# Kernel optimization log

Measured on AMD Instinct MI355X. Metric: run time of the kernel, lower is better.

The kernel has to match this reference:

```python
import jax, jax.numpy as jnp
import numpy as np

N = 100000      # num nodes == input_dim (featureless RGCN)
S = 50          # support (num relations)
B = 30          # num_bases
OUT = 16        # output_dim
E = 20000       # edges per relation


def setup_inputs() -> dict:
    key = jax.random.key(0)
    k1, k2, k3, k4, k5, k6 = jax.random.split(key, 6)
    features = jax.random.normal(k1, (N, 1), dtype=jnp.float32)
    src = jax.random.randint(k2, (S, E), 0, N, dtype=jnp.int32)
    dst = jax.random.randint(k3, (S, E), 0, N, dtype=jnp.int32)
    vals = jax.random.uniform(k4, (S, E), dtype=jnp.float32)
    # learned params (xavier-ish scale)
    W = jax.random.normal(k5, (N * B, OUT), dtype=jnp.float32) * (2.0 / (N * B + OUT)) ** 0.5
    W_comp = jax.random.normal(k6, (S, B), dtype=jnp.float32) * (2.0 / (S + B)) ** 0.5
    return {"features": features, "src": src, "dst": dst, "vals": vals, "W": W, "W_comp": W_comp}


def reference(features, src, dst, vals, W, W_comp):
    n = features.shape[0]  # == N (featureless: input_dim == num_nodes)
    # Basis decomposition, exactly as torch:
    # V = W_comp @ W.reshape(B, N, OUT).permute(1, 0, 2)  -> [N, S, OUT]
    Wb = W.reshape(B, n, OUT).transpose(1, 0, 2)          # [N, B, OUT]
    V = jnp.einsum('sb,nbo->nso', W_comp, Wb)             # [N, S, OUT]
    # torch reshape (support*input_dim, OUT): row k = node*S + rel (node-major)
    V2 = V.reshape(S * n, OUT)                            # [S*N, OUT]
    # supports is block-concat sparse [N, S*N], column = rel*N + node (relation-major)
    # output = supports @ V2: for edge (i=src, j=dst) in relation r:
    #   out[i] += val * V2[r*N + j]
    gather_idx = (jnp.arange(S, dtype=src.dtype)[:, None] * n + dst).reshape(-1)  # [S*E]
    msgs = V2[gather_idx] * vals.reshape(-1, 1)           # [S*E, OUT]
    out = jax.ops.segment_sum(msgs, src.reshape(-1), num_segments=n)  # [N, OUT]
    # featureless dropout scaling: tmp = dropout(ones(N)); p=0 -> identity
    return jax.nn.relu(out)
```

## Files before the change

### kernel.cpp

```cpp
#include <hip/hip_runtime.h>

constexpr int S_REL = 50;
constexpr int B_BASES = 30;
constexpr int OUT_DIM = 16;
constexpr int NXCD = 8;
constexpr int EDGES_PER_BLOCK = 64;

__global__ __launch_bounds__(256) void relu_inplace_kernel(float4* __restrict__ p, int n4) {
    int i = blockIdx.x * blockDim.x + threadIdx.x;
    int stride = gridDim.x * blockDim.x;
    for (; i < n4; i += stride) {
        float4 v = p[i];
        v.x = fmaxf(v.x, 0.f);
        v.y = fmaxf(v.y, 0.f);
        v.z = fmaxf(v.z, 0.f);
        v.w = fmaxf(v.w, 0.f);
        p[i] = v;
    }
}

__global__ __launch_bounds__(256) void rgcn_edge_kernel(
    const int* __restrict__ src, const int* __restrict__ dst,
    const float* __restrict__ vals, const float* __restrict__ W,
    const float* __restrict__ Wcomp, float* __restrict__ out,
    int N, int E, int nEdges, int chunksPerXcd, int nChunks) {
    __shared__ float wc[S_REL * B_BASES];
    for (int i = threadIdx.x; i < S_REL * B_BASES; i += blockDim.x)
        wc[i] = Wcomp[i];
    __syncthreads();

    const int x = blockIdx.x % NXCD;
    const int j = blockIdx.x / NXCD;
    const int chunk = x * chunksPerXcd + j;
    if (chunk >= nChunks) return;

    const int edge = chunk * EDGES_PER_BLOCK + (threadIdx.x >> 2);
    const int o4 = (threadIdx.x & 3) * 4;
    if (edge >= nEdges) return;

    const int r = edge / E;
    const int d = dst[edge];
    const int s = src[edge];
    const float v = vals[edge];

    const int k = r * N + d;
    const int node = k / S_REL;
    const int rel = k - node * S_REL;

    const float* wp = W + (size_t)node * OUT_DIM + o4;
    const size_t bstride = (size_t)N * OUT_DIM;
    const float* wcr = wc + rel * B_BASES;

    float c[B_BASES];
#pragma unroll
    for (int b = 0; b < B_BASES; ++b) c[b] = wcr[b];

    float4 acc = make_float4(0.f, 0.f, 0.f, 0.f);
#pragma unroll
    for (int b = 0; b < B_BASES; ++b) {
        float4 w4 = *reinterpret_cast<const float4*>(wp + (size_t)b * bstride);
        acc.x = fmaf(c[b], w4.x, acc.x);
        acc.y = fmaf(c[b], w4.y, acc.y);
        acc.z = fmaf(c[b], w4.z, acc.z);
        acc.w = fmaf(c[b], w4.w, acc.w);
    }

    float* op = out + (size_t)s * OUT_DIM + o4;
    atomicAdd(op + 0, v * acc.x);
    atomicAdd(op + 1, v * acc.y);
    atomicAdd(op + 2, v * acc.z);
    atomicAdd(op + 3, v * acc.w);
}

extern "C" void kernel_launch(void* const* d_in, const int* in_sizes, int n_in,
                              void* d_out, int out_size, void* d_ws, size_t ws_size,
                              hipStream_t stream) {
    const int* src = (const int*)d_in[1];
    const int* dst = (const int*)d_in[2];
    const float* vals = (const float*)d_in[3];
    const float* W = (const float*)d_in[4];
    const float* Wcomp = (const float*)d_in[5];
    float* out = (float*)d_out;

    const int N = in_sizes[0];
    const int nEdges = in_sizes[1];
    const int E = nEdges / S_REL;

    hipMemsetAsync(d_out, 0, (size_t)out_size * sizeof(float), stream);

    const int nChunks = (nEdges + EDGES_PER_BLOCK - 1) / EDGES_PER_BLOCK;
    const int chunksPerXcd = (nChunks + NXCD - 1) / NXCD;
    const int eblocks = chunksPerXcd * NXCD;
    rgcn_edge_kernel<<<eblocks, 256, 0, stream>>>(src, dst, vals, W, Wcomp, out,
                                                  N, E, nEdges, chunksPerXcd, nChunks);

    const int n4 = out_size / 4;
    int zb = (n4 + 255) / 256;
    const int rblocks = zb < 2048 ? zb : 2048;
    relu_inplace_kernel<<<rblocks, 256, 0, stream>>>((float4*)out, n4);
}
```

Before: 486.4 us.

## Replace float atomics with histogram-scan bucketing and per-node segmented reduction

Replaces per-edge float atomicAdds into the output with a CSR-style pipeline. A histogram counts edges per source node, a single-block scan builds offsets, and a gather kernel writes each edge's message into a bucketed workspace slot. A reduce kernel then sums each node's messages and applies ReLU in one pass. This removes the output memset, the float atomics and the separate ReLU pass, at the cost of five launches, a serial single-block scan over 100k nodes, and a 64 MB message buffer round trip.

```diff
diff --git a/kernel.cpp b/kernel.cpp
--- a/kernel.cpp
+++ b/kernel.cpp
@@ -11,65 +11,149 @@
     int stride = gridDim.x * blockDim.x;
     for (; i < n4; i += stride) {
         float4 v = p[i];
-        v.x = fmaxf(v.x, 0.f);
-        v.y = fmaxf(v.y, 0.f);
-        v.z = fmaxf(v.z, 0.f);
-        v.w = fmaxf(v.w, 0.f);
+        v.x = fmaxf(v.x, 0.f); v.y = fmaxf(v.y, 0.f);
+        v.z = fmaxf(v.z, 0.f); v.w = fmaxf(v.w, 0.f);
         p[i] = v;
     }
 }
 
-__global__ __launch_bounds__(256) void rgcn_edge_kernel(
+__global__ __launch_bounds__(256) void rgcn_edge_atomic_kernel(
     const int* __restrict__ src, const int* __restrict__ dst,
     const float* __restrict__ vals, const float* __restrict__ W,
     const float* __restrict__ Wcomp, float* __restrict__ out,
     int N, int E, int nEdges, int chunksPerXcd, int nChunks) {
     __shared__ float wc[S_REL * B_BASES];
-    for (int i = threadIdx.x; i < S_REL * B_BASES; i += blockDim.x)
-        wc[i] = Wcomp[i];
+    for (int i = threadIdx.x; i < S_REL * B_BASES; i += blockDim.x) wc[i] = Wcomp[i];
     __syncthreads();
-
     const int x = blockIdx.x % NXCD;
     const int j = blockIdx.x / NXCD;
     const int chunk = x * chunksPerXcd + j;
     if (chunk >= nChunks) return;
-
     const int edge = chunk * EDGES_PER_BLOCK + (threadIdx.x >> 2);
     const int o4 = (threadIdx.x & 3) * 4;
     if (edge >= nEdges) return;
-
     const int r = edge / E;
     const int d = dst[edge];
     const int s = src[edge];
     const float v = vals[edge];
-
     const int k = r * N + d;
     const int node = k / S_REL;
     const int rel = k - node * S_REL;
-
     const float* wp = W + (size_t)node * OUT_DIM + o4;
     const size_t bstride = (size_t)N * OUT_DIM;
     const float* wcr = wc + rel * B_BASES;
-
-    float c[B_BASES];
-#pragma unroll
-    for (int b = 0; b < B_BASES; ++b) c[b] = wcr[b];
-
     float4 acc = make_float4(0.f, 0.f, 0.f, 0.f);
 #pragma unroll
     for (int b = 0; b < B_BASES; ++b) {
         float4 w4 = *reinterpret_cast<const float4*>(wp + (size_t)b * bstride);
-        acc.x = fmaf(c[b], w4.x, acc.x);
-        acc.y = fmaf(c[b], w4.y, acc.y);
-        acc.z = fmaf(c[b], w4.z, acc.z);
-        acc.w = fmaf(c[b], w4.w, acc.w);
-    }
-
+        float c = wcr[b];
+        acc.x = fmaf(c, w4.x, acc.x); acc.y = fmaf(c, w4.y, acc.y);
+        acc.z = fmaf(c, w4.z, acc.z); acc.w = fmaf(c, w4.w, acc.w);
+    }
     float* op = out + (size_t)s * OUT_DIM + o4;
-    atomicAdd(op + 0, v * acc.x);
-    atomicAdd(op + 1, v * acc.y);
-    atomicAdd(op + 2, v * acc.z);
-    atomicAdd(op + 3, v * acc.w);
+    atomicAdd(op + 0, v * acc.x); atomicAdd(op + 1, v * acc.y);
+    atomicAdd(op + 2, v * acc.z); atomicAdd(op + 3, v * acc.w);
+}
+
+__global__ __launch_bounds__(256) void hist_kernel(
+    const int* __restrict__ src, unsigned* __restrict__ cnt, int nEdges) {
+    int i = blockIdx.x * blockDim.x + threadIdx.x;
+    int stride = gridDim.x * blockDim.x;
+    for (; i < nEdges; i += stride) atomicAdd(&cnt[src[i]], 1u);
+}
+
+__global__ __launch_bounds__(1024) void scan_kernel(
+    const unsigned* __restrict__ cnt, unsigned* __restrict__ offs,
+    unsigned* __restrict__ cur, int N) {
+    __shared__ unsigned sums[1024];
+    const int t = threadIdx.x;
+    const int per = (N + 1023) / 1024;
+    const int lo = t * per;
+    const int hi = (lo + per < N) ? lo + per : N;
+    unsigned s = 0;
+    for (int i = lo; i < hi; ++i) s += cnt[i];
+    sums[t] = s;
+    __syncthreads();
+    for (int d = 1; d < 1024; d <<= 1) {
+        unsigned v = (t >= d) ? sums[t - d] : 0u;
+        __syncthreads();
+        sums[t] += v;
+        __syncthreads();
+    }
+    unsigned base = (t == 0) ? 0u : sums[t - 1];
+    for (int i = lo; i < hi; ++i) {
+        unsigned c = cnt[i];
+        offs[i] = base;
+        cur[i] = base;
+        base += c;
+    }
+    if (t == 1023) offs[N] = sums[1023];
+}
+
+__global__ __launch_bounds__(256) void gather_kernel(
+    const int* __restrict__ src, const int* __restrict__ dst,
+    const float* __restrict__ vals, const float* __restrict__ W,
+    const float* __restrict__ Wcomp, float* __restrict__ msgs,
+    unsigned* __restrict__ cur,
+    int N, int E, int nEdges, int chunksPerXcd, int nChunks) {
+    __shared__ float wc[S_REL * B_BASES];
+    for (int i = threadIdx.x; i < S_REL * B_BASES; i += blockDim.x) wc[i] = Wcomp[i];
+    __syncthreads();
+
+    const int x = blockIdx.x % NXCD;
+    const int j = blockIdx.x / NXCD;
+    const int chunk = x * chunksPerXcd + j;
+    if (chunk >= nChunks) return;
+    const int edge = chunk * EDGES_PER_BLOCK + (threadIdx.x >> 2);
+    const int o4 = (threadIdx.x & 3) * 4;
+    if (edge >= nEdges) return;
+
+    const int r = edge / E;
+    const int d = dst[edge];
+    const int s = src[edge];
+    const float v = vals[edge];
+    const int k = r * N + d;
+    const int node = k / S_REL;
+    const int rel = k - node * S_REL;
+
+    const float* wp = W + (size_t)node * OUT_DIM + o4;
+    const size_t bstride = (size_t)N * OUT_DIM;
+    const float* wcr = wc + rel * B_BASES;
+
+    float4 acc = make_float4(0.f, 0.f, 0.f, 0.f);
+#pragma unroll
+    for (int b = 0; b < B_BASES; ++b) {
+        float4 w4 = *reinterpret_cast<const float4*>(wp + (size_t)b * bstride);
+        float c = wcr[b];
+        acc.x = fmaf(c, w4.x, acc.x); acc.y = fmaf(c, w4.y, acc.y);
+        acc.z = fmaf(c, w4.z, acc.z); acc.w = fmaf(c, w4.w, acc.w);
+    }
+
+    unsigned pos = 0;
+    if ((threadIdx.x & 3) == 0) pos = atomicAdd(&cur[s], 1u);
+    pos = __shfl(pos, 0, 4);
+
+    float4* mp = reinterpret_cast<float4*>(msgs + (size_t)pos * OUT_DIM);
+    mp[threadIdx.x & 3] = make_float4(v * acc.x, v * acc.y, v * acc.z, v * acc.w);
+}
+
+__global__ __launch_bounds__(256) void reduce_kernel(
+    const float* __restrict__ msgs, const unsigned* __restrict__ offs,
+    float* __restrict__ out, int N) {
+    const int t = blockIdx.x * blockDim.x + threadIdx.x;
+    const int n = t >> 2;
+    const int q = t & 3;
+    if (n >= N) return;
+    const unsigned b = offs[n];
+    const unsigned e = offs[n + 1];
+    float4 acc = make_float4(0.f, 0.f, 0.f, 0.f);
+    for (unsigned p = b; p < e; ++p) {
+        float4 m = *reinterpret_cast<const float4*>(msgs + (size_t)p * OUT_DIM + q * 4);
+        acc.x += m.x; acc.y += m.y; acc.z += m.z; acc.w += m.w;
+    }
+    float4* op = reinterpret_cast<float4*>(out + (size_t)n * OUT_DIM);
+    op[q] = make_float4(fmaxf(acc.x, 0.f), fmaxf(acc.y, 0.f),
+                        fmaxf(acc.z, 0.f), fmaxf(acc.w, 0.f));
 }
 
 extern "C" void kernel_launch(void* const* d_in, const int* in_sizes, int n_in,
@@ -86,16 +170,38 @@
     const int nEdges = in_sizes[1];
     const int E = nEdges / S_REL;
 
-    hipMemsetAsync(d_out, 0, (size_t)out_size * sizeof(float), stream);
-
     const int nChunks = (nEdges + EDGES_PER_BLOCK - 1) / EDGES_PER_BLOCK;
     const int chunksPerXcd = (nChunks + NXCD - 1) / NXCD;
     const int eblocks = chunksPerXcd * NXCD;
-    rgcn_edge_kernel<<<eblocks, 256, 0, stream>>>(src, dst, vals, W, Wcomp, out,
-                                                  N, E, nEdges, chunksPerXcd, nChunks);
-
-    const int n4 = out_size / 4;
-    int zb = (n4 + 255) / 256;
-    const int rblocks = zb < 2048 ? zb : 2048;
-    relu_inplace_kernel<<<rblocks, 256, 0, stream>>>((float4*)out, n4);
-}
+
+    const size_t msgsBytes = (size_t)nEdges * OUT_DIM * sizeof(float);
+    const size_t needed = msgsBytes + (size_t)(3 * N + 1) * sizeof(unsigned);
+
+    if (ws_size < needed) {
+        hipMemsetAsync(d_out, 0, (size_t)out_size * sizeof(float), stream);
+        rgcn_edge_atomic_kernel<<<eblocks, 256, 0, stream>>>(
+            src, dst, vals, W, Wcomp, out, N, E, nEdges, chunksPerXcd, nChunks);
+        const int n4 = out_size / 4;
+        int zb = (n4 + 255) / 256;
+        relu_inplace_kernel<<<(zb < 2048 ? zb : 2048), 256, 0, stream>>>((float4*)out, n4);
+        return;
+    }
+
+    float* msgs = (float*)d_ws;
+    unsigned* cnt = (unsigned*)((char*)d_ws + msgsBytes);
+    unsigned* offs = cnt + N;
+    unsigned* cur = offs + N + 1;
+
+    hipMemsetAsync(cnt, 0, (size_t)N * sizeof(unsigned), stream);
+
+    int hb = (nEdges + 255) / 256;
+    hist_kernel<<<(hb < 2048 ? hb : 2048), 256, 0, stream>>>(src, cnt, nEdges);
+
+    scan_kernel<<<1, 1024, 0, stream>>>(cnt, offs, cur, N);
+
+    gather_kernel<<<eblocks, 256, 0, stream>>>(src, dst, vals, W, Wcomp, msgs, cur,
+                                               N, E, nEdges, chunksPerXcd, nChunks);
+
+    const int rblocks = (N * 4 + 255) / 256;
+    reduce_kernel<<<rblocks, 256, 0, stream>>>(msgs, offs, out, N);
+}
```

Measured after the change: 752.2 us. 54.6% more time.

## Materialize basis-combined V2 in relation chunks, then gather-scatter per edge

Applied to the files above, without the earlier changes.

Instead of recombining the 30 basis weight rows on the fly for every edge, each group of up to 10 relations now gets its dense V2 rows written to workspace by a coalesced build kernel. A separate consume kernel then gathers one 16-float row per edge and atomically adds it into the output. The goal is to replace scattered 30-way W gathers per edge with streaming reads of W. The cost is computing all N*S rows rather than only the rows edges touch, plus extra workspace writes and more kernel launches. The old fused path remains as a fallback when the workspace is too small.

```diff
diff --git a/kernel.cpp b/kernel.cpp
--- a/kernel.cpp
+++ b/kernel.cpp
@@ -3,57 +3,28 @@
 constexpr int S_REL = 50;
 constexpr int B_BASES = 30;
 constexpr int OUT_DIM = 16;
-constexpr int NXCD = 8;
-constexpr int EDGES_PER_BLOCK = 64;
 
-__global__ __launch_bounds__(256) void relu_inplace_kernel(float4* __restrict__ p, int n4) {
-    int i = blockIdx.x * blockDim.x + threadIdx.x;
-    int stride = gridDim.x * blockDim.x;
-    for (; i < n4; i += stride) {
-        float4 v = p[i];
-        v.x = fmaxf(v.x, 0.f);
-        v.y = fmaxf(v.y, 0.f);
-        v.z = fmaxf(v.z, 0.f);
-        v.w = fmaxf(v.w, 0.f);
-        p[i] = v;
-    }
-}
 
-__global__ __launch_bounds__(256) void rgcn_edge_kernel(
-    const int* __restrict__ src, const int* __restrict__ dst,
-    const float* __restrict__ vals, const float* __restrict__ W,
-    const float* __restrict__ Wcomp, float* __restrict__ out,
-    int N, int E, int nEdges, int chunksPerXcd, int nChunks) {
+__global__ __launch_bounds__(256) void build_v2_kernel(
+    const float* __restrict__ W, const float* __restrict__ Wcomp,
+    float* __restrict__ V2c, int kBase, int rows, int N) {
     __shared__ float wc[S_REL * B_BASES];
     for (int i = threadIdx.x; i < S_REL * B_BASES; i += blockDim.x)
         wc[i] = Wcomp[i];
     __syncthreads();
 
-    const int x = blockIdx.x % NXCD;
-    const int j = blockIdx.x / NXCD;
-    const int chunk = x * chunksPerXcd + j;
-    if (chunk >= nChunks) return;
+    int t = blockIdx.x * blockDim.x + threadIdx.x;
+    int idx = t >> 2;
+    int o4 = (t & 3) * 4;
+    if (idx >= rows) return;
 
-    const int edge = chunk * EDGES_PER_BLOCK + (threadIdx.x >> 2);
-    const int o4 = (threadIdx.x & 3) * 4;
-    if (edge >= nEdges) return;
-
-    const int r = edge / E;
-    const int d = dst[edge];
-    const int s = src[edge];
-    const float v = vals[edge];
-
-    const int k = r * N + d;
-    const int node = k / S_REL;
-    const int rel = k - node * S_REL;
+    int k = kBase + idx;
+    int node = k / S_REL;
+    int rel = k - node * S_REL;
 
     const float* wp = W + (size_t)node * OUT_DIM + o4;
     const size_t bstride = (size_t)N * OUT_DIM;
-    const float* wcr = wc + rel * B_BASES;
-
-    float c[B_BASES];
-#pragma unroll
-    for (int b = 0; b < B_BASES; ++b) c[b] = wcr[b];
+    const float* c = wc + rel * B_BASES;
 
     float4 acc = make_float4(0.f, 0.f, 0.f, 0.f);
 #pragma unroll
@@ -64,12 +35,80 @@
         acc.z = fmaf(c[b], w4.z, acc.z);
         acc.w = fmaf(c[b], w4.w, acc.w);
     }
+    *reinterpret_cast<float4*>(V2c + (size_t)idx * OUT_DIM + o4) = acc;
+}
 
+__global__ __launch_bounds__(256) void consume_kernel(
+    const int* __restrict__ src, const int* __restrict__ dst,
+    const float* __restrict__ vals, const float* __restrict__ V2c,
+    float* __restrict__ out,
+    int kBase, int edgeBase, int nEdgesChunk, int N, int E) {
+    int t = blockIdx.x * blockDim.x + threadIdx.x;
+    int el = t >> 4;
+    int o = t & 15;
+    if (el >= nEdgesChunk) return;
+    int edge = edgeBase + el;
+
+    int r = edge / E;
+    int d = dst[edge];
+    int s = src[edge];
+    float v = vals[edge];
+
+    int row = r * N + d - kBase;
+    float m = v * V2c[(size_t)row * OUT_DIM + o];
+    atomicAdd(out + (size_t)s * OUT_DIM + o, m);
+}
+
+__global__ __launch_bounds__(256) void relu_inplace_kernel(float4* __restrict__ p, int n4) {
+    int i = blockIdx.x * blockDim.x + threadIdx.x;
+    int stride = gridDim.x * blockDim.x;
+    for (; i < n4; i += stride) {
+        float4 v = p[i];
+        v.x = fmaxf(v.x, 0.f); v.y = fmaxf(v.y, 0.f);
+        v.z = fmaxf(v.z, 0.f); v.w = fmaxf(v.w, 0.f);
+        p[i] = v;
+    }
+}
+
+constexpr int NXCD = 8;
+constexpr int EDGES_PER_BLOCK = 64;
+
+__global__ __launch_bounds__(256) void rgcn_edge_atomic_kernel(
+    const int* __restrict__ src, const int* __restrict__ dst,
+    const float* __restrict__ vals, const float* __restrict__ W,
+    const float* __restrict__ Wcomp, float* __restrict__ out,
+    int N, int E, int nEdges, int chunksPerXcd, int nChunks) {
+    __shared__ float wc[S_REL * B_BASES];
+    for (int i = threadIdx.x; i < S_REL * B_BASES; i += blockDim.x) wc[i] = Wcomp[i];
+    __syncthreads();
+    const int x = blockIdx.x % NXCD;
+    const int j = blockIdx.x / NXCD;
+    const int chunk = x * chunksPerXcd + j;
+    if (chunk >= nChunks) return;
+    const int edge = chunk * EDGES_PER_BLOCK + (threadIdx.x >> 2);
+    const int o4 = (threadIdx.x & 3) * 4;
+    if (edge >= nEdges) return;
+    const int r = edge / E;
+    const int d = dst[edge];
+    const int s = src[edge];
+    const float v = vals[edge];
+    const int k = r * N + d;
+    const int node = k / S_REL;
+    const int rel = k - node * S_REL;
+    const float* wp = W + (size_t)node * OUT_DIM + o4;
+    const size_t bstride = (size_t)N * OUT_DIM;
+    const float* wcr = wc + rel * B_BASES;
+    float4 acc = make_float4(0.f, 0.f, 0.f, 0.f);
+#pragma unroll
+    for (int b = 0; b < B_BASES; ++b) {
+        float4 w4 = *reinterpret_cast<const float4*>(wp + (size_t)b * bstride);
+        float c = wcr[b];
+        acc.x = fmaf(c, w4.x, acc.x); acc.y = fmaf(c, w4.y, acc.y);
+        acc.z = fmaf(c, w4.z, acc.z); acc.w = fmaf(c, w4.w, acc.w);
+    }
     float* op = out + (size_t)s * OUT_DIM + o4;
-    atomicAdd(op + 0, v * acc.x);
-    atomicAdd(op + 1, v * acc.y);
-    atomicAdd(op + 2, v * acc.z);
-    atomicAdd(op + 3, v * acc.w);
+    atomicAdd(op + 0, v * acc.x); atomicAdd(op + 1, v * acc.y);
+    atomicAdd(op + 2, v * acc.z); atomicAdd(op + 3, v * acc.w);
 }
 
 extern "C" void kernel_launch(void* const* d_in, const int* in_sizes, int n_in,
@@ -88,14 +127,35 @@
 
     hipMemsetAsync(d_out, 0, (size_t)out_size * sizeof(float), stream);
 
-    const int nChunks = (nEdges + EDGES_PER_BLOCK - 1) / EDGES_PER_BLOCK;
-    const int chunksPerXcd = (nChunks + NXCD - 1) / NXCD;
-    const int eblocks = chunksPerXcd * NXCD;
-    rgcn_edge_kernel<<<eblocks, 256, 0, stream>>>(src, dst, vals, W, Wcomp, out,
-                                                  N, E, nEdges, chunksPerXcd, nChunks);
+    const size_t relBytes = (size_t)N * OUT_DIM * sizeof(float);
+    int cap = (int)(ws_size / relBytes);
+    int Rc = cap < 10 ? cap : 10;
+    if (Rc > S_REL) Rc = S_REL;
+
+    if (Rc < 1) {
+        const int nChunks = (nEdges + EDGES_PER_BLOCK - 1) / EDGES_PER_BLOCK;
+        const int chunksPerXcd = (nChunks + NXCD - 1) / NXCD;
+        rgcn_edge_atomic_kernel<<<chunksPerXcd * NXCD, 256, 0, stream>>>(
+            src, dst, vals, W, Wcomp, out, N, E, nEdges, chunksPerXcd, nChunks);
+    } else {
+        float* V2c = (float*)d_ws;
+        for (int r0 = 0; r0 < S_REL; r0 += Rc) {
+            const int rc = (r0 + Rc <= S_REL) ? Rc : (S_REL - r0);
+            const int rows = rc * N;
+            const int kBase = r0 * N;
+            const int edgeBase = r0 * E;
+            const int nEdgesChunk = rc * E;
+
+            const int bblocks = (rows * 4 + 255) / 256;
+            build_v2_kernel<<<bblocks, 256, 0, stream>>>(W, Wcomp, V2c, kBase, rows, N);
+
+            const int cblocks = (nEdgesChunk * 16 + 255) / 256;
+            consume_kernel<<<cblocks, 256, 0, stream>>>(src, dst, vals, V2c, out,
+                                                        kBase, edgeBase, nEdgesChunk, N, E);
+        }
+    }
 
     const int n4 = out_size / 4;
     int zb = (n4 + 255) / 256;
-    const int rblocks = zb < 2048 ? zb : 2048;
-    relu_inplace_kernel<<<rblocks, 256, 0, stream>>>((float4*)out, n4);
+    relu_inplace_kernel<<<(zb < 2048 ? zb : 2048), 256, 0, stream>>>((float4*)out, n4);
 }
```

Result: slower. 820.3 us (+68.6%).

## Materialize basis-combined V2 densely and replace float atomics with CSR segmented reduce

Applied to the files above, without the earlier changes.

Each call now builds the full [N*S, OUT] relation weight table with a tiled kernel that reads W once and combines the bases for all 50 relations. The per-edge 30-basis random gathers are replaced by a single 64-byte row gather. Float atomics into the output are replaced by a counting sort on src (histogram, three-stage scan, scatter of messages) and an atomic-free per-node reduction with ReLU fused in. The cost is a large dense V2 write, several small kernel launches, and a workspace requirement; if the workspace is too small the code falls back to the old atomic path.

```diff
diff --git a/kernel.cpp b/kernel.cpp
--- a/kernel.cpp
+++ b/kernel.cpp
@@ -3,6 +3,132 @@
 constexpr int S_REL = 50;
 constexpr int B_BASES = 30;
 constexpr int OUT_DIM = 16;
+constexpr int TILE_N = 32;
+
+__global__ __launch_bounds__(128) void build_v2_tiled(
+    const float4* __restrict__ W4, const float* __restrict__ Wcomp,
+    float4* __restrict__ V24, int N) {
+    __shared__ float scw[S_REL * B_BASES];
+    const int t = threadIdx.x;
+    const int nodeBase = blockIdx.x * TILE_N;
+    const int nf4 = N * 4;
+
+    for (int i = t; i < S_REL * B_BASES; i += 128) scw[i] = Wcomp[i];
+
+    float4 f[B_BASES];
+    const int off = nodeBase * 4 + t;
+#pragma unroll
+    for (int b = 0; b < B_BASES; ++b)
+        f[b] = (off < nf4) ? W4[(size_t)b * nf4 + off]
+                           : make_float4(0.f, 0.f, 0.f, 0.f);
+    __syncthreads();
+
+    const int nl = t >> 2;
+    const int o4 = t & 3;
+    const int node = nodeBase + nl;
+    if (node >= N) return;
+
+    for (int rel = 0; rel < S_REL; ++rel) {
+        const float* c = &scw[rel * B_BASES];
+        float4 a = make_float4(0.f, 0.f, 0.f, 0.f);
+#pragma unroll
+        for (int b = 0; b < B_BASES; ++b) {
+            float cb = c[b];
+            a.x = fmaf(cb, f[b].x, a.x);
+            a.y = fmaf(cb, f[b].y, a.y);
+            a.z = fmaf(cb, f[b].z, a.z);
+            a.w = fmaf(cb, f[b].w, a.w);
+        }
+        V24[((size_t)node * S_REL + rel) * 4 + o4] = a;
+    }
+}
+
+__global__ __launch_bounds__(256) void hist_kernel(
+    const int* __restrict__ src, unsigned* __restrict__ cnt, int nEdges) {
+    int i = blockIdx.x * blockDim.x + threadIdx.x;
+    int stride = gridDim.x * blockDim.x;
+    for (; i < nEdges; i += stride) atomicAdd(&cnt[src[i]], 1u);
+}
+
+__global__ __launch_bounds__(1024) void scanA_kernel(
+    const unsigned* __restrict__ cnt, unsigned* __restrict__ offs,
+    unsigned* __restrict__ bsum, int N) {
+    __shared__ unsigned s[1024];
+    const int t = threadIdx.x;
+    const int i = blockIdx.x * 1024 + t;
+    unsigned x = (i < N) ? cnt[i] : 0u;
+    s[t] = x;
+    __syncthreads();
+    for (int d = 1; d < 1024; d <<= 1) {
+        unsigned v = (t >= d) ? s[t - d] : 0u;
+        __syncthreads();
+        s[t] += v;
+        __syncthreads();
+    }
+    if (i < N) offs[i] = s[t] - x;
+    if (t == 1023) bsum[blockIdx.x] = s[1023];
+}
+
+__global__ __launch_bounds__(64) void scanB_kernel(
+    unsigned* __restrict__ bsum, unsigned* __restrict__ bofs, int nb) {
+    if (threadIdx.x == 0) {
+        unsigned run = 0;
+        for (int j = 0; j < nb; ++j) { unsigned x = bsum[j]; bofs[j] = run; run += x; }
+    }
+}
+
+__global__ __launch_bounds__(1024) void scanC_kernel(
+    unsigned* __restrict__ offs, unsigned* __restrict__ cur,
+    const unsigned* __restrict__ bofs, int N, int nEdges) {
+    const int i = blockIdx.x * 1024 + threadIdx.x;
+    if (i < N) {
+        unsigned o = offs[i] + bofs[i >> 10];
+        offs[i] = o;
+        cur[i] = o;
+    }
+    if (i == 0) offs[N] = (unsigned)nEdges;
+}
+
+__global__ __launch_bounds__(256) void consume_kernel(
+    const int* __restrict__ src, const int* __restrict__ dst,
+    const float* __restrict__ vals, const float4* __restrict__ V24,
+    float4* __restrict__ M4, unsigned* __restrict__ cur,
+    int N, int E, int nEdges) {
+    int t = blockIdx.x * blockDim.x + threadIdx.x;
+    int e = t >> 2;
+    int q = t & 3;
+    if (e >= nEdges) return;
+    int r = e / E;
+    int d = dst[e];
+    int s = src[e];
+    float v = vals[e];
+    int k = r * N + d;
+    float4 g = V24[(size_t)k * 4 + q];
+    float4 m = make_float4(v * g.x, v * g.y, v * g.z, v * g.w);
+    unsigned pos = 0;
+    if (q == 0) pos = atomicAdd(&cur[s], 1u);
+    pos = __shfl(pos, 0, 4);
+    M4[(size_t)pos * 4 + q] = m;
+}
+
+__global__ __launch_bounds__(256) void reduce_kernel(
+    const float4* __restrict__ M4, const unsigned* __restrict__ offs,
+    float4* __restrict__ out4, int N) {
+    int t = blockIdx.x * blockDim.x + threadIdx.x;
+    int n = t >> 2;
+    int q = t & 3;
+    if (n >= N) return;
+    unsigned b = offs[n];
+    unsigned e = offs[n + 1];
+    float4 a = make_float4(0.f, 0.f, 0.f, 0.f);
+    for (unsigned p = b; p < e; ++p) {
+        float4 m = M4[(size_t)p * 4 + q];
+        a.x += m.x; a.y += m.y; a.z += m.z; a.w += m.w;
+    }
+    out4[(size_t)n * 4 + q] = make_float4(fmaxf(a.x, 0.f), fmaxf(a.y, 0.f),
+                                          fmaxf(a.z, 0.f), fmaxf(a.w, 0.f));
+}
+
 constexpr int NXCD = 8;
 constexpr int EDGES_PER_BLOCK = 64;
 
@@ -11,65 +137,48 @@
     int stride = gridDim.x * blockDim.x;
     for (; i < n4; i += stride) {
         float4 v = p[i];
-        v.x = fmaxf(v.x, 0.f);
-        v.y = fmaxf(v.y, 0.f);
-        v.z = fmaxf(v.z, 0.f);
-        v.w = fmaxf(v.w, 0.f);
+        v.x = fmaxf(v.x, 0.f); v.y = fmaxf(v.y, 0.f);
+        v.z = fmaxf(v.z, 0.f); v.w = fmaxf(v.w, 0.f);
         p[i] = v;
     }
 }
 
-__global__ __launch_bounds__(256) void rgcn_edge_kernel(
+__global__ __launch_bounds__(256) void rgcn_edge_atomic_kernel(
     const int* __restrict__ src, const int* __restrict__ dst,
     const float* __restrict__ vals, const float* __restrict__ W,
     const float* __restrict__ Wcomp, float* __restrict__ out,
     int N, int E, int nEdges, int chunksPerXcd, int nChunks) {
     __shared__ float wc[S_REL * B_BASES];
-    for (int i = threadIdx.x; i < S_REL * B_BASES; i += blockDim.x)
-        wc[i] = Wcomp[i];
+    for (int i = threadIdx.x; i < S_REL * B_BASES; i += blockDim.x) wc[i] = Wcomp[i];
     __syncthreads();
-
     const int x = blockIdx.x % NXCD;
     const int j = blockIdx.x / NXCD;
     const int chunk = x * chunksPerXcd + j;
     if (chunk >= nChunks) return;
-
     const int edge = chunk * EDGES_PER_BLOCK + (threadIdx.x >> 2);
     const int o4 = (threadIdx.x & 3) * 4;
     if (edge >= nEdges) return;
-
     const int r = edge / E;
     const int d = dst[edge];
     const int s = src[edge];
     const float v = vals[edge];
-
     const int k = r * N + d;
     const int node = k / S_REL;
     const int rel = k - node * S_REL;
-
     const float* wp = W + (size_t)node * OUT_DIM + o4;
     const size_t bstride = (size_t)N * OUT_DIM;
     const float* wcr = wc + rel * B_BASES;
-
-    float c[B_BASES];
-#pragma unroll
-    for (int b = 0; b < B_BASES; ++b) c[b] = wcr[b];
-
     float4 acc = make_float4(0.f, 0.f, 0.f, 0.f);
 #pragma unroll
     for (int b = 0; b < B_BASES; ++b) {
         float4 w4 = *reinterpret_cast<const float4*>(wp + (size_t)b * bstride);
-        acc.x = fmaf(c[b], w4.x, acc.x);
-        acc.y = fmaf(c[b], w4.y, acc.y);
-        acc.z = fmaf(c[b], w4.z, acc.z);
-        acc.w = fmaf(c[b], w4.w, acc.w);
-    }
-
+        float c = wcr[b];
+        acc.x = fmaf(c, w4.x, acc.x); acc.y = fmaf(c, w4.y, acc.y);
+        acc.z = fmaf(c, w4.z, acc.z); acc.w = fmaf(c, w4.w, acc.w);
+    }
     float* op = out + (size_t)s * OUT_DIM + o4;
-    atomicAdd(op + 0, v * acc.x);
-    atomicAdd(op + 1, v * acc.y);
-    atomicAdd(op + 2, v * acc.z);
-    atomicAdd(op + 3, v * acc.w);
+    atomicAdd(op + 0, v * acc.x); atomicAdd(op + 1, v * acc.y);
+    atomicAdd(op + 2, v * acc.z); atomicAdd(op + 3, v * acc.w);
 }
 
 extern "C" void kernel_launch(void* const* d_in, const int* in_sizes, int n_in,
@@ -80,22 +189,52 @@
     const float* vals = (const float*)d_in[3];
     const float* W = (const float*)d_in[4];
     const float* Wcomp = (const float*)d_in[5];
-    float* out = (float*)d_out;
 
     const int N = in_sizes[0];
     const int nEdges = in_sizes[1];
     const int E = nEdges / S_REL;
 
-    hipMemsetAsync(d_out, 0, (size_t)out_size * sizeof(float), stream);
-
-    const int nChunks = (nEdges + EDGES_PER_BLOCK - 1) / EDGES_PER_BLOCK;
-    const int chunksPerXcd = (nChunks + NXCD - 1) / NXCD;
-    const int eblocks = chunksPerXcd * NXCD;
-    rgcn_edge_kernel<<<eblocks, 256, 0, stream>>>(src, dst, vals, W, Wcomp, out,
-                                                  N, E, nEdges, chunksPerXcd, nChunks);
-
-    const int n4 = out_size / 4;
-    int zb = (n4 + 255) / 256;
-    const int rblocks = zb < 2048 ? zb : 2048;
-    relu_inplace_kernel<<<rblocks, 256, 0, stream>>>((float4*)out, n4);
-}
+    const int nbScan = (N + 1023) / 1024;
+    const size_t v2Bytes = (size_t)S_REL * N * OUT_DIM * sizeof(float);
+    const size_t msgBytes = (size_t)nEdges * OUT_DIM * sizeof(float);
+    const size_t intBytes = ((size_t)3 * N + 1 + 2 * nbScan) * sizeof(unsigned);
+    const size_t needed = v2Bytes + msgBytes + intBytes;
+
+    if (ws_size < needed) {
+        float* out = (float*)d_out;
+        hipMemsetAsync(d_out, 0, (size_t)out_size * sizeof(float), stream);
+        const int nChunks = (nEdges + EDGES_PER_BLOCK - 1) / EDGES_PER_BLOCK;
+        const int chunksPerXcd = (nChunks + NXCD - 1) / NXCD;
+        rgcn_edge_atomic_kernel<<<chunksPerXcd * NXCD, 256, 0, stream>>>(
+            src, dst, vals, W, Wcomp, out, N, E, nEdges, chunksPerXcd, nChunks);
+        const int n4 = out_size / 4;
+        int zb = (n4 + 255) / 256;
+        relu_inplace_kernel<<<(zb < 2048 ? zb : 2048), 256, 0, stream>>>((float4*)out, n4);
+        return;
+    }
+
+    float4* V24 = (float4*)d_ws;
+    float4* M4 = (float4*)((char*)d_ws + v2Bytes);
+    unsigned* cnt = (unsigned*)((char*)d_ws + v2Bytes + msgBytes);
+    unsigned* offs = cnt + N;
+    unsigned* cur = offs + N + 1;
+    unsigned* bsum = cur + N;
+    unsigned* bofs = bsum + nbScan;
+
+    const int bblocks = (N + TILE_N - 1) / TILE_N;
+    build_v2_tiled<<<bblocks, 128, 0, stream>>>((const float4*)W, Wcomp, V24, N);
+
+    hipMemsetAsync(cnt, 0, (size_t)N * sizeof(unsigned), stream);
+    int hb = (nEdges + 255) / 256;
+    hist_kernel<<<(hb < 2048 ? hb : 2048), 256, 0, stream>>>(src, cnt, nEdges);
+    scanA_kernel<<<nbScan, 1024, 0, stream>>>(cnt, offs, bsum, N);
+    scanB_kernel<<<1, 64, 0, stream>>>(bsum, bofs, nbScan);
+    scanC_kernel<<<nbScan, 1024, 0, stream>>>(offs, cur, bofs, N, nEdges);
+
+    const long long cthreads = (long long)nEdges * 4;
+    consume_kernel<<<(int)((cthreads + 255) / 256), 256, 0, stream>>>(
+        src, dst, vals, V24, M4, cur, N, E, nEdges);
+
+    const int rblocks = (N * 4 + 255) / 256;
+    reduce_kernel<<<rblocks, 256, 0, stream>>>(M4, offs, (float4*)d_out, N);
+}
```

After: 586.6 us. 20.6% more time.
